# Optimization experiments

Measured on AMD Instinct MI355X. Metric: run time of the kernel, lower is better.

Reference implementation:

```python
import jax, jax.numpy as jnp
import numpy as np

B, L, NC, D = 4, 2048, 4096, 128
ITERS = 4
NHEAD = 8
T = L // 2
C2 = 2 * D


def _ln(x, g, b, eps=1e-5):
    m = jnp.mean(x, axis=-1, keepdims=True)
    v = jnp.var(x, axis=-1, keepdims=True)
    return (x - m) * jax.lax.rsqrt(v + eps) * g + b


def _mlp3(x, W1, b1, W2, b2, W3, b3):
    h = jax.nn.relu(x @ W1 + b1)
    h = jax.nn.relu(h @ W2 + b2)
    return h @ W3 + b3


def _lstm(inp, h, c, Wih, Whh, gi, bi, gh, bh, gc, bc):
    gates = _ln(inp @ Wih, gi, bi) + _ln(h @ Whh, gh, bh)
    i, f, g, o = jnp.split(gates, 4, axis=-1)
    cy = _ln(jax.nn.sigmoid(f) * c + jax.nn.sigmoid(i) * jnp.tanh(g), gc, bc)
    hy = jax.nn.sigmoid(o) * jnp.tanh(cy)
    return hy, cy


def _flip(x):
    # flip matrix with full literal counts == permutation swapping pos/neg halves
    half = x.shape[1] // 2
    return jnp.concatenate([x[:, half:], x[:, :half]], axis=1)


def setup_inputs():
    key = jax.random.key(0)
    ks = iter(jax.random.split(key, 64))
    def xav(fi, fo):
        s = float(np.sqrt(6.0 / (fi + fo)))
        return jax.random.uniform(next(ks), (fi, fo), jnp.float32, -s, s)
    def rn(*shape):
        return jax.random.normal(next(ks), shape, jnp.float32)
    inp = {}
    inp['adjacency_matrices'] = (jax.random.uniform(next(ks), (B, L, NC)) < 0.03).astype(jnp.float32)
    inp['batch_lit_counts'] = jnp.full((B,), L, dtype=jnp.int32)
    inp['L_init'] = rn(1, D) / np.sqrt(D).astype(np.float32)
    inp['C_init'] = rn(1, D) / np.sqrt(D).astype(np.float32)
    for p in ('LC', 'CL'):
        for i in (1, 2, 3):
            inp[p + '_W' + str(i)] = xav(D, D)
            inp[p + '_b' + str(i)] = jnp.full((D,), 0.01, jnp.float32)
    for p, isz in (('Lu', 2 * D), ('Cu', D)):
        inp[p + '_Wih'] = rn(isz, 4 * D)  # torch uses raw randn for LSTM weights
        inp[p + '_Whh'] = rn(D, 4 * D)
        for ln, n in (('lni', 4 * D), ('lnh', 4 * D), ('lnc', D)):
            inp[p + '_' + ln + '_g'] = jnp.ones((n,), jnp.float32)
            inp[p + '_' + ln + '_b'] = jnp.zeros((n,), jnp.float32)
    for p in ('k', 'q', 'v'):
        inp['att_W' + p] = xav(C2, C2)
        inp['att_b' + p] = jnp.zeros((C2,), jnp.float32)
    for p in ('asn', 'vote'):
        inp[p + '_W1'] = xav(C2, D)
        inp[p + '_b1'] = jnp.full((D,), 0.01, jnp.float32)
        inp[p + '_W2'] = xav(D, 1)
        inp[p + '_b2'] = jnp.full((1,), 0.01, jnp.float32)
    return inp


def reference(adjacency_matrices, batch_lit_counts, L_init, C_init,
              LC_W1, LC_b1, LC_W2, LC_b2, LC_W3, LC_b3,
              CL_W1, CL_b1, CL_W2, CL_b2, CL_W3, CL_b3,
              Lu_Wih, Lu_Whh, Lu_lni_g, Lu_lni_b, Lu_lnh_g, Lu_lnh_b, Lu_lnc_g, Lu_lnc_b,
              Cu_Wih, Cu_Whh, Cu_lni_g, Cu_lni_b, Cu_lnh_g, Cu_lnh_b, Cu_lnc_g, Cu_lnc_b,
              att_Wk, att_bk, att_Wq, att_bq, att_Wv, att_bv,
              asn_W1, asn_b1, asn_W2, asn_b2, vote_W1, vote_b1, vote_W2, vote_b2):
    A = adjacency_matrices
    Bb, Ll, Cc = A.shape
    Lh = jnp.broadcast_to(L_init, (Bb, Ll, D))
    Lc = jnp.zeros_like(Lh)
    Ch = jnp.broadcast_to(C_init, (Bb, Cc, D))
    Cxc = jnp.zeros_like(Ch)
    for _ in range(ITERS):
        # literal -> clause messages (gather via A^T)
        LC = jnp.einsum('blc,bld->bcd', A, _mlp3(Lh, LC_W1, LC_b1, LC_W2, LC_b2, LC_W3, LC_b3))
        Ch, Cxc = _lstm(LC, Ch, Cxc, Cu_Wih, Cu_Whh, Cu_lni_g, Cu_lni_b, Cu_lnh_g, Cu_lnh_b, Cu_lnc_g, Cu_lnc_b)
        # clause -> literal messages (scatter via A)
        CL = jnp.einsum('blc,bcd->bld', A, _mlp3(Ch, CL_W1, CL_b1, CL_W2, CL_b2, CL_W3, CL_b3))
        Lh, Lc = _lstm(jnp.concatenate([CL, _flip(Lh)], axis=-1), Lh, Lc,
                       Lu_Wih, Lu_Whh, Lu_lni_g, Lu_lni_b, Lu_lnh_g, Lu_lnh_b, Lu_lnc_g, Lu_lnc_b)
    # readout [h_l ; h_{~l}], positive literals only
    read = jnp.concatenate([Lh, _flip(Lh)], axis=-1)[:, :T]  # [B,T,2D]
    half = batch_lit_counts // 2
    mask = (jnp.arange(T)[None, :] < half[:, None]).astype(read.dtype)  # [B,T]
    read = read * mask[:, :, None]
    hd = C2 // NHEAD
    def heads(x, W, b):
        return (x @ W + b).reshape(Bb, T, NHEAD, hd).transpose(0, 2, 1, 3)
    k = heads(read, att_Wk, att_bk)
    q = heads(read, att_Wq, att_bq)
    v = heads(read, att_Wv, att_bv)
    att = jnp.einsum('bhtd,bhsd->bhts', q, k) * (1.0 / np.sqrt(hd))
    sq = (mask[:, None, :, None] * mask[:, None, None, :]) > 0  # [B,1,T,T]
    att = jnp.where(sq, att, -jnp.inf)
    att = jax.nn.softmax(att, axis=-1)
    att = jnp.where(jnp.isnan(att), 0.0, att)
    y = jnp.einsum('bhts,bhsd->bhtd', att, v).transpose(0, 2, 1, 3).reshape(Bb, T, C2)
    def head_mlp(x, W1, b1, W2, b2):
        return jax.nn.sigmoid(jax.nn.relu(x @ W1 + b1) @ W2 + b2)[..., 0]
    assignments = head_mlp(y, asn_W1, asn_b1, asn_W2, asn_b2) * mask  # [B,T]
    vote_vals = head_mlp(y, vote_W1, vote_b1, vote_W2, vote_b2)
    votes = jnp.sum(vote_vals * mask, axis=1) / jnp.maximum(jnp.sum(mask, axis=1), 1.0)
    return votes, assignments
```

## Files before the change

kernel.cpp:

```cpp
#include <hip/hip_runtime.h>


#define B_    4
#define L_    2048
#define NC_   4096
#define D_    128
#define ITERS_ 4
#define NH_   8
#define T_    1024
#define C2_   256
#define HD_   32
#define BL_   (B_*L_)
#define BNC_  (B_*NC_)
#define QS_   768

typedef unsigned short u16;
typedef __attribute__((ext_vector_type(8))) short b16x8;
typedef __attribute__((ext_vector_type(4))) float f32x4;

static __device__ __forceinline__ float bf2f(u16 u){
  union{unsigned int i; float f;} x; x.i = ((unsigned int)u) << 16; return x.f;
}
static __device__ __forceinline__ u16 f2bf(float f){
  union{float f; unsigned int i;} x; x.f = f;
  unsigned int r = x.i + 0x7fffu + ((x.i >> 16) & 1u);
  return (u16)(r >> 16);
}
static __device__ __forceinline__ float sigm(float x){ return 1.f/(1.f+expf(-x)); }
static __device__ __forceinline__ void split2(float v, u16& h, u16& l){
  unsigned bits = __float_as_uint(v);
  u16 hb = (u16)(bits >> 16);
  float hf = __uint_as_float(((unsigned)hb) << 16);
  h = hb; l = f2bf(v - hf);
}

__global__ __launch_bounds__(256) void k_detect(const unsigned int* __restrict__ a,
                                                int* __restrict__ flag){
  int bad = 0;
  for (int i = threadIdx.x; i < 32768; i += 256){
    unsigned int w = a[i];
    if (w != 0u && w != 0x3F800000u) bad = 1;
  }
  __shared__ int s[256];
  s[threadIdx.x] = bad; __syncthreads();
  for (int o = 128; o > 0; o >>= 1){
    if (threadIdx.x < o) s[threadIdx.x] |= s[threadIdx.x + o];
    __syncthreads();
  }
  if (threadIdx.x == 0) *flag = s[0];
}

#define NCJ_ 29
struct CJobs { const void* src[NCJ_]; unsigned n[NCJ_]; unsigned off[NCJ_]; };

__global__ __launch_bounds__(256) void k_cvt_all(CJobs jb, float* __restrict__ pool,
                                                 const int* __restrict__ flag){
  int j = blockIdx.y;
  unsigned n = jb.n[j];
  unsigned i = blockIdx.x*256 + threadIdx.x;
  if (i >= n) return;
  float v;
  if (*flag) v = bf2f(((const u16*)jb.src[j])[i]);
  else       v = ((const float*)jb.src[j])[i];
  pool[jb.off[j] + i] = v;
}

#define NPJ_ 16
struct PJobs { const void* src[NPJ_]; unsigned n[NPJ_], N[NPJ_], koff[NPJ_],
               ksb[NPJ_], dh[NPJ_], dl[NPJ_]; };

__global__ __launch_bounds__(256) void k_prep(PJobs pj, u16* __restrict__ up,
                                              const int* __restrict__ flag){
  int jj = blockIdx.y;
  unsigned n = pj.n[jj];
  unsigned g = blockIdx.x*256 + threadIdx.x;
  if (g >= n) return;
  unsigned j = g & 7, lane = (g>>3)&63;
  unsigned ksb = pj.ksb[jj];
  unsigned ks = (g>>9) & ((1u<<ksb)-1u);
  unsigned nt = g >> (9+ksb);
  unsigned ncol = nt*16 + (lane&15);
  unsigned k = pj.koff[jj] + ks*32 + ((lane>>4)&3)*8 + j;
  unsigned si = k*pj.N[jj] + ncol;
  float v;
  if (*flag) v = bf2f(((const u16*)pj.src[jj])[si]);
  else       v = ((const float*)pj.src[jj])[si];
  u16 h,l; split2(v, h, l);
  up[pj.dh[jj] + g] = h;
  up[pj.dl[jj] + g] = l;
}

__global__ __launch_bounds__(256) void k_init(float* __restrict__ h, float* __restrict__ c,
                                              const float* __restrict__ init, int n){
  int i = blockIdx.x*256 + threadIdx.x;
  if (i < n){ h[i] = init[i & (D_-1)]; c[i] = 0.f; }
}

__global__ void k_zero_u(unsigned* __restrict__ p, int n){
  int i = blockIdx.x*256 + threadIdx.x; if (i < n) p[i] = 0u;
}
__global__ void k_zero(float* p, int n){
// ... 81 lines not shown
    atomicAdd(cnt_c + cb + j, 1u);
  }
}

__global__ __launch_bounds__(256) void k_fill_c(const unsigned* __restrict__ bits,
    const unsigned* __restrict__ off_c, unsigned* __restrict__ cur_c,
    u16* __restrict__ val_c){
  int g = blockIdx.x*256 + threadIdx.x;
  unsigned m = bits[g];
  int row = g >> 7, w = g & 127;
  int b = row >> 11, l = row & (L_-1);
  unsigned cb = ((unsigned)b << 12) + w*32;
  while (m){
    int j = __ffs(m) - 1; m &= m - 1;
    unsigned idx = cb + j;
    unsigned pos = atomicAdd(cur_c + idx, 1u);
    val_c[off_c[idx] + pos] = (u16)l;
  }
}

__global__ __launch_bounds__(256) void k_spmm(const unsigned* __restrict__ off,
    const u16* __restrict__ val, const float* __restrict__ M, float* __restrict__ out,
    int sh1, int sh2){
  int row  = blockIdx.x*4 + (threadIdx.x >> 6);
  int lane = threadIdx.x & 63;
  unsigned p0 = off[row], p1 = off[row+1];
  const float2* Mp = (const float2*)M + (((size_t)(row >> sh1) << sh2) * 64) + lane;
  float x = 0.f, y = 0.f;
  for (unsigned p = p0; p < p1; ++p){
    float2 v = Mp[(size_t)val[p] * 64];
    x += v.x; y += v.y;
  }
  float2 r; r.x = x; r.y = y;
  ((float2*)out)[(size_t)row*64 + lane] = r;
}

__global__ __launch_bounds__(512) void k_mlp3m(const float* __restrict__ X,
    const u16* __restrict__ W1h, const u16* __restrict__ W1l,
    const u16* __restrict__ W2h, const u16* __restrict__ W2l,
    const u16* __restrict__ W3h, const u16* __restrict__ W3l,
    const float* __restrict__ b1, const float* __restrict__ b2,
    const float* __restrict__ b3, float* __restrict__ Y)
{
  __shared__ __align__(16) u16 Ah[32*136];
  __shared__ __align__(16) u16 Al[32*136];
  const int tid = threadIdx.x, lane = tid & 63, wv = tid >> 6;
  const int quad = lane >> 4, l15 = lane & 15;
  const int r0 = blockIdx.x * 32;
  {
    int row = tid >> 4, c0 = (tid & 15)*8;
    const float4* src = (const float4*)(X + (size_t)(r0+row)*128 + c0);
    float4 v0 = src[0], v1 = src[1];
    u16 h,l;
    split2(v0.x,h,l); Ah[row*136+c0]  =h; Al[row*136+c0]  =l;
    split2(v0.y,h,l); Ah[row*136+c0+1]=h; Al[row*136+c0+1]=l;
    split2(v0.z,h,l); Ah[row*136+c0+2]=h; Al[row*136+c0+2]=l;
    split2(v0.w,h,l); Ah[row*136+c0+3]=h; Al[row*136+c0+3]=l;
    split2(v1.x,h,l); Ah[row*136+c0+4]=h; Al[row*136+c0+4]=l;
    split2(v1.y,h,l); Ah[row*136+c0+5]=h; Al[row*136+c0+5]=l;
    split2(v1.z,h,l); Ah[row*136+c0+6]=h; Al[row*136+c0+6]=l;
    split2(v1.w,h,l); Ah[row*136+c0+7]=h; Al[row*136+c0+7]=l;
  }
  __syncthreads();
  const u16* Whs[3] = {W1h, W2h, W3h};
  const u16* Wls[3] = {W1l, W2l, W3l};
  const float* bs[3] = {b1, b2, b3};
  #pragma unroll
  for (int layer = 0; layer < 3; layer++){
    f32x4 acc[2] = {};
    #pragma unroll
    for (int ks = 0; ks < 4; ks++){
      b16x8 a_h[2], a_l[2];
      #pragma unroll
      for (int mt = 0; mt < 2; mt++){
        int ao = (mt*16 + l15)*136 + ks*32 + quad*8;
        a_h[mt] = *(const b16x8*)(Ah + ao);
        a_l[mt] = *(const b16x8*)(Al + ao);
      }
      size_t bo = (size_t)((wv*4 + ks)*64 + lane)*8;
      b16x8 bh = *(const b16x8*)(Whs[layer] + bo);
      b16x8 bl = *(const b16x8*)(Wls[layer] + bo);
      #pragma unroll
      for (int mt = 0; mt < 2; mt++){
        acc[mt] = __builtin_amdgcn_mfma_f32_16x16x32_bf16(a_h[mt], bh, acc[mt],0,0,0);
        acc[mt] = __builtin_amdgcn_mfma_f32_16x16x32_bf16(a_h[mt], bl, acc[mt],0,0,0);
        acc[mt] = __builtin_amdgcn_mfma_f32_16x16x32_bf16(a_l[mt], bh, acc[mt],0,0,0);
      }
    }
    int col = wv*16 + l15;
    if (layer < 2){
      float bb = bs[layer][col];
      __syncthreads();
      #pragma unroll
      for (int mt = 0; mt < 2; mt++)
        #pragma unroll
        for (int r = 0; r < 4; r++){
          int row = mt*16 + quad*4 + r;
          float v = fmaxf(acc[mt][r] + bb, 0.f);
          u16 h,l; split2(v,h,l);
          Ah[row*136 + col] = h; Al[row*136 + col] = l;
        }
      __syncthreads();
    } else {
      float bb = bs[2][col];
      #pragma unroll
      for (int mt = 0; mt < 2; mt++)
        #pragma unroll
        for (int r = 0; r < 4; r++){
          int row = mt*16 + quad*4 + r;
          Y[(size_t)(r0+row)*128 + col] = acc[mt][r] + bb;
        }
    }
  }
}

template<int NSEG>
__global__ __launch_bounds__(512) void k_lstm_mfma(
    const float* __restrict__ A0, const float* __restrict__ A1, const float* __restrict__ A2,
    int flip1,
    const u16* __restrict__ W0h, const u16* __restrict__ W0l,
    const u16* __restrict__ W1h, const u16* __restrict__ W1l,
    const u16* __restrict__ W2h, const u16* __restrict__ W2l,
    const float* __restrict__ lni_g, const float* __restrict__ lni_b,
    const float* __restrict__ lnh_g, const float* __restrict__ lnh_b,
    const float* __restrict__ lnc_g, const float* __restrict__ lnc_b,
    const float* __restrict__ c_in, float* __restrict__ c_out,
    float* __restrict__ h_out)
{
  __shared__ __align__(16) float G[32*516];
  __shared__ float red[8][32][4];
  __shared__ float st[32][4];
  u16* Ah = (u16*)G;
  u16* Al = Ah + 32*136;
  const int tid = threadIdx.x, lane = tid & 63, wv = tid >> 6;
  const int quad = lane >> 4, l15 = lane & 15;
  const int r0 = blockIdx.x * 32;

  f32x4 acc1[2][4] = {}, acc2[2][4] = {};

  #pragma unroll
  for (int s = 0; s < NSEG; ++s){
    const float* Ap = (s==0) ? A0 : ((s==1) ? A1 : A2);
    const u16* Wh = (s==0) ? W0h : ((s==1) ? W1h : W2h);
    const u16* Wl = (s==0) ? W0l : ((s==1) ? W1l : W2l);
    const int fm = (s==1) ? flip1 : 0;
    __syncthreads();
    {
      int row = tid >> 4, c0 = (tid & 15)*8;
      int arow = (r0 + row) ^ fm;
      const float4* src = (const float4*)(Ap + (size_t)arow*128 + c0);
      float4 v0 = src[0], v1 = src[1];
      u16 h,l;
      split2(v0.x,h,l); Ah[row*136+c0]  =h; Al[row*136+c0]  =l;
      split2(v0.y,h,l); Ah[row*136+c0+1]=h; Al[row*136+c0+1]=l;
      split2(v0.z,h,l); Ah[row*136+c0+2]=h; Al[row*136+c0+2]=l;
      split2(v0.w,h,l); Ah[row*136+c0+3]=h; Al[row*136+c0+3]=l;
      split2(v1.x,h,l); Ah[row*136+c0+4]=h; Al[row*136+c0+4]=l;
      split2(v1.y,h,l); Ah[row*136+c0+5]=h; Al[row*136+c0+5]=l;
      split2(v1.z,h,l); Ah[row*136+c0+6]=h; Al[row*136+c0+6]=l;
      split2(v1.w,h,l); Ah[row*136+c0+7]=h; Al[row*136+c0+7]=l;
    }
    __syncthreads();
    f32x4 (*accp)[4] = (s == NSEG-1) ? acc2 : acc1;
    #pragma unroll
    for (int ks = 0; ks < 4; ks++){
      b16x8 a_h[2], a_l[2];
      #pragma unroll
      for (int mt = 0; mt < 2; mt++){
        int ao = (mt*16 + l15)*136 + ks*32 + quad*8;
        a_h[mt] = *(const b16x8*)(Ah + ao);
        a_l[mt] = *(const b16x8*)(Al + ao);
      }
      #pragma unroll
      for (int ntl = 0; ntl < 4; ntl++){
        int nt = wv*4 + ntl;
        size_t bo = (size_t)((nt*4 + ks)*64 + lane)*8;
        b16x8 bh = *(const b16x8*)(Wh + bo);
        b16x8 bl = *(const b16x8*)(Wl + bo);
        #pragma unroll
        for (int mt = 0; mt < 2; mt++){
          accp[mt][ntl] = __builtin_amdgcn_mfma_f32_16x16x32_bf16(a_h[mt], bh, accp[mt][ntl],0,0,0);
          accp[mt][ntl] = __builtin_amdgcn_mfma_f32_16x16x32_bf16(a_h[mt], bl, accp[mt][ntl],0,0,0);
          accp[mt][ntl] = __builtin_amdgcn_mfma_f32_16x16x32_bf16(a_l[mt], bh, accp[mt][ntl],0,0,0);
        }
      }
    }
  }

  #pragma unroll
  for (int mt = 0; mt < 2; mt++)
    #pragma unroll
    for (int r = 0; r < 4; r++){
      float s1=0.f, q1=0.f, s2=0.f, q2=0.f;
      #pragma unroll
      for (int ntl = 0; ntl < 4; ntl++){
        float v1 = acc1[mt][ntl][r]; s1 += v1; q1 += v1*v1;
        float v2 = acc2[mt][ntl][r]; s2 += v2; q2 += v2*v2;
      }
      #pragma unroll
      for (int m = 1; m < 16; m <<= 1){
        s1 += __shfl_xor(s1, m); q1 += __shfl_xor(q1, m);
        s2 += __shfl_xor(s2, m); q2 += __shfl_xor(q2, m);
      }
      if (l15 == 0){
        int row = mt*16 + quad*4 + r;
        red[wv][row][0]=s1; red[wv][row][1]=q1; red[wv][row][2]=s2; red[wv][row][3]=q2;
      }
    }
  __syncthreads();
  if (tid < 32){
    int row = tid;
    float s1=0.f,q1=0.f,s2=0.f,q2=0.f;
    #pragma unroll
    for (int w = 0; w < 8; w++){
      s1 += red[w][row][0]; q1 += red[w][row][1];
      s2 += red[w][row][2]; q2 += red[w][row][3];
    }
    const float i512 = 1.f/512.f;
    float m1 = s1*i512, v1 = fmaxf(q1*i512 - m1*m1, 0.f);
    float m2 = s2*i512, v2 = fmaxf(q2*i512 - m2*m2, 0.f);
    st[row][0] = m1; st[row][1] = rsqrtf(v1 + 1e-5f);
    st[row][2] = m2; st[row][3] = rsqrtf(v2 + 1e-5f);
  }
  __syncthreads();

  #pragma unroll
  for (int mt = 0; mt < 2; mt++)
    #pragma unroll
    for (int ntl = 0; ntl < 4; ntl++){
      int col = wv*64 + ntl*16 + l15;
      float gi = lni_g[col], bi = lni_b[col];
      float gh = lnh_g[col], bh = lnh_b[col];
      #pragma unroll
      for (int r = 0; r < 4; r++){
        int row = mt*16 + quad*4 + r;
        float v = (acc1[mt][ntl][r] - st[row][0])*st[row][1]*gi + bi
                + (acc2[mt][ntl][r] - st[row][2])*st[row][3]*gh + bh;
        G[row*516 + col] = v;
      }
    }
  __syncthreads();

  float lcg0 = lnc_g[lane], lcb0 = lnc_b[lane];
  float lcg1 = lnc_g[lane+64], lcb1 = lnc_b[lane+64];
  const float i128 = 1.f/128.f;
  #pragma unroll
  for (int i = 0; i < 4; i++){
    int row = wv*4 + i;
    int rg = r0 + row;
    float cp[2], sc = 0.f, qc = 0.f;
    #pragma unroll
    for (int jj = 0; jj < 2; jj++){
      int c = lane + 64*jj;
      float iv = sigm(G[row*516 + c]);
      float fv = sigm(G[row*516 + 128 + c]);
      float gv = tanhf(G[row*516 + 256 + c]);
      cp[jj] = fv * c_in[(size_t)rg*128 + c] + iv*gv;
      sc += cp[jj]; qc += cp[jj]*cp[jj];
    }
    #pragma unroll
    for (int m = 1; m < 64; m <<= 1){ sc += __shfl_xor(sc, m); qc += __shfl_xor(qc, m); }
    float mc = sc*i128, vc = fmaxf(qc*i128 - mc*mc, 0.f), rsc = rsqrtf(vc + 1e-5f);
    #pragma unroll
    for (int jj = 0; jj < 2; jj++){
      int c = lane + 64*jj;
      float cy = (cp[jj]-mc)*rsc*(jj ? lcg1 : lcg0) + (jj ? lcb1 : lcb0);
      c_out[(size_t)rg*128 + c] = cy;
      float ov = sigm(G[row*516 + 384 + c]);
      h_out[(size_t)rg*128 + c] = ov*tanhf(cy);
    }
  }
}

template<int NT, int NSPLIT, int KK32, int ACT, int GATHER>
__global__ __launch_bounds__(512) void k_gemm_mfma(const float* __restrict__ A,
    const u16* __restrict__ Wh, const u16* __restrict__ Wl,
    const float* __restrict__ bias, float* __restrict__ Y,
    const int* __restrict__ counts)
{
  const int NTOT = NSPLIT*8*NT*16;
  const int LDA = KK32*32 + 8;
  __shared__ __align__(16) u16 Ah[32*(KK32*32+8)];
  __shared__ __align__(16) u16 Al[32*(KK32*32+8)];
  const int tid = threadIdx.x, lane = tid & 63, wv = tid >> 6;
  const int quad = lane >> 4, l15 = lane & 15;
  const int r0 = blockIdx.x * 32, by = blockIdx.y;
  {
    int row = tid >> 4, c0 = (tid & 15)*(KK32*2);
    if (GATHER){
      int r = r0 + row; int b = r >> 10; int t = r & 1023;
      int half = counts[b] / 2; if (half > T_) half = T_;
      float msk = (t < half) ? 1.f : 0.f;
      #pragma unroll
      for (int q4 = 0; q4 < KK32/2; q4++){
        int c = c0 + q4*4;
        const float* src = A + ((size_t)(b*L_ + t + ((c >= 128) ? T_ : 0))*128 + (c & 127));
        float4 v = *(const float4*)src;
        u16 h,l;
        split2(v.x*msk,h,l); Ah[row*LDA+c]  =h; Al[row*LDA+c]  =l;
        split2(v.y*msk,h,l); Ah[row*LDA+c+1]=h; Al[row*LDA+c+1]=l;
        split2(v.z*msk,h,l); Ah[row*LDA+c+2]=h; Al[row*LDA+c+2]=l;
        split2(v.w*msk,h,l); Ah[row*LDA+c+3]=h; Al[row*LDA+c+3]=l;
      }
    } else {
      const float4* src = (const float4*)(A + (size_t)(r0+row)*(KK32*32) + c0);
      #pragma unroll
      for (int q4 = 0; q4 < KK32/2; q4++){
        float4 v = src[q4]; int c = c0 + q4*4;
        u16 h,l;
        split2(v.x,h,l); Ah[row*LDA+c]  =h; Al[row*LDA+c]  =l;
        split2(v.y,h,l); Ah[row*LDA+c+1]=h; Al[row*LDA+c+1]=l;
        split2(v.z,h,l); Ah[row*LDA+c+2]=h; Al[row*LDA+c+2]=l;
        split2(v.w,h,l); Ah[row*LDA+c+3]=h; Al[row*LDA+c+3]=l;
      }
    }
  }
  __syncthreads();
  f32x4 acc[2][NT] = {};
  #pragma unroll
  for (int ks = 0; ks < KK32; ks++){
    b16x8 a_h[2], a_l[2];
    #pragma unroll
    for (int mt = 0; mt < 2; mt++){
      int ao = (mt*16 + l15)*LDA + ks*32 + quad*8;
      a_h[mt] = *(const b16x8*)(Ah + ao);
      a_l[mt] = *(const b16x8*)(Al + ao);
    }
    #pragma unroll
    for (int ntl = 0; ntl < NT; ntl++){
      int nt = by*(8*NT) + wv*NT + ntl;
      size_t bo = (size_t)((nt*KK32 + ks)*64 + lane)*8;
      b16x8 bh = *(const b16x8*)(Wh + bo);
      b16x8 bl = *(const b16x8*)(Wl + bo);
      #pragma unroll
      for (int mt = 0; mt < 2; mt++){
        acc[mt][ntl] = __builtin_amdgcn_mfma_f32_16x16x32_bf16(a_h[mt], bh, acc[mt][ntl],0,0,0);
        acc[mt][ntl] = __builtin_amdgcn_mfma_f32_16x16x32_bf16(a_h[mt], bl, acc[mt][ntl],0,0,0);
        acc[mt][ntl] = __builtin_amdgcn_mfma_f32_16x16x32_bf16(a_l[mt], bh, acc[mt][ntl],0,0,0);
      }
    }
  }
  #pragma unroll
  for (int mt = 0; mt < 2; mt++)
    #pragma unroll
    for (int ntl = 0; ntl < NT; ntl++){
      int colg = by*(8*NT*16) + wv*(NT*16) + ntl*16 + l15;
      float bb = bias[colg];
      #pragma unroll
      for (int r = 0; r < 4; r++){
        int row = mt*16 + quad*4 + r;
        float v = acc[mt][ntl][r] + bb;
        if (ACT) v = fmaxf(v, 0.f);
        Y[(size_t)(r0+row)*NTOT + colg] = v;
      }
    }
}

__global__ __launch_bounds__(256) void k_attn_tile(const float* __restrict__ qkv,
    const int* __restrict__ counts, float* __restrict__ y)
{
  const int b = blockIdx.z, h = blockIdx.y, t0 = blockIdx.x*64;
  int half = counts[b] / 2; if (half > T_) half = T_; if (half < 0) half = 0;
  const int tid = threadIdx.x;
  const int lane = tid & 63, wv = tid >> 6;
  const int lr = tid >> 2, lc = (tid & 3)*8;

  if (t0 >= half){
    float* yp = y + ((size_t)(b*T_ + t0 + lr)*C2_ + h*HD_ + lc);
    #pragma unroll
    for (int j = 0; j < 8; j++) yp[j] = 0.f;
    return;
  }

  __shared__ float Qs[64][36];
  __shared__ float Ks[64][32];
  __shared__ float Ss[64][68];

  {
    const float* qp = qkv + (size_t)(b*T_ + t0 + lr)*QS_ + h*HD_ + lc;
    float4 a0 = *(const float4*)qp;
    float4 a1 = *(const float4*)(qp+4);
    *(float4*)&Qs[lr][lc]   = a0;
    *(float4*)&Qs[lr][lc+4] = a1;
  }

  const int ty = tid >> 4, tx = tid & 15;
  const int sr = wv*16 + (lane & 15);
  const int spart = (lane >> 4) * 16;
  const int rp = lane >> 3, cq = lane & 7;
  const int r0 = wv*16 + rp*2;

  float4 acc0 = {0.f,0.f,0.f,0.f}, acc1 = {0.f,0.f,0.f,0.f};
  float mst = -3e38f, lst = 0.f;
  const float scale = 0.17677669529663687f;
  const int nt = (half + 63) >> 6;

  for (int st = 0; st < nt; ++st){
    const int s0 = st*64;
    __syncthreads();
    {
      const float* kp = qkv + (size_t)(b*T_ + s0 + lr)*QS_ + 256 + h*HD_ + lc;
      float4 k0 = *(const float4*)kp;
      float4 k1 = *(const float4*)(kp+4);
      int key = (lr >> 2) & 7;
      int c0 = lc >> 2;
      *(float4*)&Ks[lr][4*((c0  ) ^ key)] = k0;
      *(float4*)&Ks[lr][4*((c0+1) ^ key)] = k1;
    }
    __syncthreads();

    float s4[4][4];
    #pragma unroll
    for (int i = 0; i < 4; i++)
      #pragma unroll
      for (int j = 0; j < 4; j++) s4[i][j] = 0.f;
    const int xk = tx & 7;
    #pragma unroll
    for (int kk4 = 0; kk4 < 8; kk4++){
      float4 a4[4], b4[4];
      #pragma unroll
      for (int i = 0; i < 4; i++) a4[i] = *(const float4*)&Qs[ty*4+i][kk4*4];
      const int pk = 4*(kk4 ^ xk);
      #pragma unroll
      for (int j = 0; j < 4; j++) b4[j] = *(const float4*)&Ks[tx*4+j][pk];
      #pragma unroll
      for (int i = 0; i < 4; i++)
        #pragma unroll
        for (int j = 0; j < 4; j++)
          s4[i][j] += a4[i].x*b4[j].x + a4[i].y*b4[j].y + a4[i].z*b4[j].z + a4[i].w*b4[j].w;
    }
    #pragma unroll
    for (int i = 0; i < 4; i++){
      float4 w4;
      w4.x = (s0 + tx*4 + 0 < half) ? s4[i][0]*scale : -1e30f;
      w4.y = (s0 + tx*4 + 1 < half) ? s4[i][1]*scale : -1e30f;
      w4.z = (s0 + tx*4 + 2 < half) ? s4[i][2]*scale : -1e30f;
      w4.w = (s0 + tx*4 + 3 < half) ? s4[i][3]*scale : -1e30f;
      *(float4*)&Ss[ty*4+i][tx*4] = w4;
    }

    float pvv[16];
    float vmax = -3e38f;
    #pragma unroll
    for (int c4 = 0; c4 < 4; c4++){
      float4 t4 = *(const float4*)&Ss[sr][spart + c4*4];
      pvv[c4*4+0] = t4.x; pvv[c4*4+1] = t4.y; pvv[c4*4+2] = t4.z; pvv[c4*4+3] = t4.w;
      vmax = fmaxf(vmax, fmaxf(fmaxf(t4.x, t4.y), fmaxf(t4.z, t4.w)));
    }
    vmax = fmaxf(vmax, __shfl_xor(vmax, 16));
    vmax = fmaxf(vmax, __shfl_xor(vmax, 32));
    float nm = fmaxf(mst, vmax);
    float alpha = expf(mst - nm);
    float psum = 0.f;
    #pragma unroll
    for (int c = 0; c < 16; c++){
      float p = expf(pvv[c] - nm);
      pvv[c] = p; psum += p;
    }
    psum += __shfl_xor(psum, 16);
    psum += __shfl_xor(psum, 32);
    lst = lst*alpha + psum;
    mst = nm;
    #pragma unroll
    for (int c4 = 0; c4 < 4; c4++){
      float4 w4; w4.x = pvv[c4*4+0]; w4.y = pvv[c4*4+1]; w4.z = pvv[c4*4+2]; w4.w = pvv[c4*4+3];
      *(float4*)&Ss[sr][spart + c4*4] = w4;
    }
    float al0 = __shfl(alpha, 2*rp);
    float al1 = __shfl(alpha, 2*rp + 1);
    acc0.x *= al0; acc0.y *= al0; acc0.z *= al0; acc0.w *= al0;
    acc1.x *= al1; acc1.y *= al1; acc1.z *= al1; acc1.w *= al1;

    const float* vbase = qkv + (size_t)(b*T_ + s0)*QS_ + 512 + h*HD_ + cq*4;
    #pragma unroll 4
    for (int kk4 = 0; kk4 < 16; kk4++){
      float4 p0 = *(const float4*)&Ss[r0  ][kk4*4];
      float4 p1 = *(const float4*)&Ss[r0+1][kk4*4];
      float4 v0 = *(const float4*)(vbase + (size_t)(kk4*4+0)*QS_);
      float4 v1 = *(const float4*)(vbase + (size_t)(kk4*4+1)*QS_);
      float4 v2 = *(const float4*)(vbase + (size_t)(kk4*4+2)*QS_);
      float4 v3 = *(const float4*)(vbase + (size_t)(kk4*4+3)*QS_);
      acc0.x += p0.x*v0.x + p0.y*v1.x + p0.z*v2.x + p0.w*v3.x;
      acc0.y += p0.x*v0.y + p0.y*v1.y + p0.z*v2.y + p0.w*v3.y;
      acc0.z += p0.x*v0.z + p0.y*v1.z + p0.z*v2.z + p0.w*v3.z;
      acc0.w += p0.x*v0.w + p0.y*v1.w + p0.z*v2.w + p0.w*v3.w;
      acc1.x += p1.x*v0.x + p1.y*v1.x + p1.z*v2.x + p1.w*v3.x;
      acc1.y += p1.x*v0.y + p1.y*v1.y + p1.z*v2.y + p1.w*v3.y;
      acc1.z += p1.x*v0.z + p1.y*v1.z + p1.z*v2.z + p1.w*v3.z;
      acc1.w += p1.x*v0.w + p1.y*v1.w + p1.z*v2.w + p1.w*v3.w;
    }
  }

  float l0 = __shfl(lst, 2*rp);
  float l1 = __shfl(lst, 2*rp + 1);
  float m0 = (t0 + r0     < half && l0 > 0.f) ? 1.f/l0 : 0.f;
  float m1 = (t0 + r0 + 1 < half && l1 > 0.f) ? 1.f/l1 : 0.f;
  float4 o0, o1;
  o0.x = acc0.x*m0; o0.y = acc0.y*m0; o0.z = acc0.z*m0; o0.w = acc0.w*m0;
  o1.x = acc1.x*m1; o1.y = acc1.y*m1; o1.z = acc1.z*m1; o1.w = acc1.w*m1;
  *(float4*)(y + ((size_t)(b*T_ + t0 + r0    )*C2_ + h*HD_ + cq*4)) = o0;
  *(float4*)(y + ((size_t)(b*T_ + t0 + r0 + 1)*C2_ + h*HD_ + cq*4)) = o1;
}

__global__ __launch_bounds__(128) void k_final(const float* __restrict__ hv,
    const float* __restrict__ aW2, const float* __restrict__ ab2,
    const float* __restrict__ vW2, const float* __restrict__ vb2,
    const int* __restrict__ counts, void* __restrict__ outv,
    float* __restrict__ vote_sum, const int* __restrict__ flag)
{
  int row = blockIdx.x, tid = threadIdx.x;
  int b = row / T_, t = row - b*T_;
  int half = counts[b] / 2; if (half > T_) half = T_;
  float pa = hv[(size_t)row*256 + tid]       * aW2[tid];
  float pv = hv[(size_t)row*256 + 128 + tid] * vW2[tid];
  #pragma unroll
  for (int off = 32; off > 0; off >>= 1){ pa += __shfl_down(pa, off); pv += __shfl_down(pv, off); }
  __shared__ float r[2][2];
  int wid = tid >> 6, lane = tid & 63;
  if (lane == 0){ r[0][wid] = pa; r[1][wid] = pv; }
  __syncthreads();
  if (tid == 0){
    float a  = sigm(r[0][0] + r[0][1] + ab2[0]);
    float vv = sigm(r[1][0] + r[1][1] + vb2[0]);
    bool mk = (t < half);
    float av = mk ? a : 0.f;
    if (*flag) ((u16*)outv)[4 + row] = f2bf(av);
    else       ((float*)outv)[4 + row] = av;
    if (mk) atomicAdd(vote_sum + b, vv);
  }
}

__global__ void k_votes(const float* __restrict__ vote_sum, const int* __restrict__ counts,
                        void* __restrict__ outv, const int* __restrict__ flag){
  int b = threadIdx.x;
  if (b < B_){
    int half = counts[b] / 2; if (half > T_) half = T_;
    float den = (float)(half > 1 ? half : 1);
    float vv = vote_sum[b] / den;
    if (*flag) ((u16*)outv)[b] = f2bf(vv);
    else       ((float*)outv)[b] = vv;
  }
}

extern "C" void kernel_launch(void* const* d_in, const int* in_sizes, int n_in,
                              void* d_out, int out_size, void* d_ws, size_t ws_size,
                              hipStream_t stream)
{
  const void* A_adj = d_in[0];
  const int* counts = (const int*)d_in[1];

  const size_t M1 = (size_t)1048576;
  const size_t NEED = (5*M1 + M1 + 2*M1 + 2*M1 + 700416 + 16416 + 8224
                       + 16384 + 8192 + 520000 + 520000 + 32) * sizeof(float);
  if (ws_size < NEED) return;

  float* ws = (float*)d_ws;
  float* R    = ws;
  float* Lc   = R + 5*M1;
  float* Ch   = Lc + M1;
  float* Cc   = Ch + 2*M1;
  float* wp   = Cc + 2*M1;
  unsigned* off_c = (unsigned*)(wp + 700416);
  unsigned* off_l = off_c + 16416;
  unsigned* cnt_c = off_l + 8224;
  unsigned* cnt_l = cnt_c + 16384;
  u16* val_c = (u16*)(cnt_l + 8192);
  u16* val_l = (u16*)((float*)val_c + 520000);
  float* tail = (float*)val_l + 520000;
  float* vote_sum = tail;
  int* flag = (int*)(tail + 8);
  unsigned* bits = (unsigned*)R;

  float* R0 = R, *R1 = R + M1, *R2 = R + 2*M1, *R3 = R + 3*M1, *R4 = R + 4*M1;

  k_detect<<<1, 256, 0, stream>>>((const unsigned int*)A_adj, flag);

  CJobs cj;
  int ncj = 0;
  unsigned off = 0;
  auto cadd = [&](int idx, unsigned n)->float*{
    cj.src[ncj] = d_in[idx]; cj.n[ncj] = n; cj.off[ncj] = off;
    float* p = wp + off; off += (n + 3u) & ~3u; ncj++; return p;
  };
  float* Linit = cadd(2, 128);
// ... 11 lines not shown
  float* bqkv = wp + off;
  cj.src[ncj]=d_in[35]; cj.n[ncj]=256; cj.off[ncj]=off;       ncj++;
  cj.src[ncj]=d_in[33]; cj.n[ncj]=256; cj.off[ncj]=off+256;   ncj++;
  cj.src[ncj]=d_in[37]; cj.n[ncj]=256; cj.off[ncj]=off+512;   ncj++;
  off += 768;
  float* bhv = wp + off;
  cj.src[ncj]=d_in[39]; cj.n[ncj]=128; cj.off[ncj]=off;       ncj++;
  cj.src[ncj]=d_in[43]; cj.n[ncj]=128; cj.off[ncj]=off+128;   ncj++;
  off += 256;
  { dim3 g(2, NCJ_); k_cvt_all<<<g, 256, 0, stream>>>(cj, wp, flag); }

  u16* up = (u16*)(wp + ((off + 3u) & ~3u));
  PJobs pj;
  int npj = 0;
  unsigned uoff = 0;
  auto padd = [&](int idx, unsigned n, unsigned Nw, unsigned koff, unsigned ksb,
                  unsigned dsth, unsigned dstl){
    pj.src[npj]=d_in[idx]; pj.n[npj]=n; pj.N[npj]=Nw; pj.koff[npj]=koff;
    pj.ksb[npj]=ksb; pj.dh[npj]=dsth; pj.dl[npj]=dstl; npj++;
  };
  auto solo = [&](int idx, unsigned n, unsigned Nw, unsigned koff, unsigned ksb,
                  const u16** h, const u16** l){
    padd(idx, n, Nw, koff, ksb, uoff, uoff + n);
    *h = up + uoff; *l = up + uoff + n; uoff += 2*n;
  };
  const u16 *lc1h,*lc1l,*lc2h,*lc2l,*lc3h,*lc3l,*cl1h,*cl1l,*cl2h,*cl2l,*cl3h,*cl3l;
  const u16 *cwih_h,*cwih_l,*cwhh_h,*cwhh_l;
  const u16 *lwa_h,*lwa_l,*lwb_h,*lwb_l,*lwhh_h,*lwhh_l;
  solo(4, 16384,128,0,2,&lc1h,&lc1l);  solo(6, 16384,128,0,2,&lc2h,&lc2l);
  solo(8, 16384,128,0,2,&lc3h,&lc3l);  solo(10,16384,128,0,2,&cl1h,&cl1l);
  solo(12,16384,128,0,2,&cl2h,&cl2l);  solo(14,16384,128,0,2,&cl3h,&cl3l);
  solo(24,65536,512,0,2,&cwih_h,&cwih_l);
  solo(25,65536,512,0,2,&cwhh_h,&cwhh_l);
  solo(16,65536,512,0,  2,&lwa_h,&lwa_l);
  solo(16,65536,512,128,2,&lwb_h,&lwb_l);
  solo(17,65536,512,0,2,&lwhh_h,&lwhh_l);
  const u16* wqkv_h = up + uoff;
  const u16* wqkv_l = up + uoff + 196608;
  padd(34, 65536, 256, 0, 3, uoff,           uoff+196608);
  padd(32, 65536, 256, 0, 3, uoff+65536,     uoff+196608+65536);
  padd(36, 65536, 256, 0, 3, uoff+131072,    uoff+196608+131072);
  uoff += 393216;
  const u16* whv_h = up + uoff;
  const u16* whv_l = up + uoff + 65536;
  padd(38, 32768, 128, 0, 3, uoff,        uoff+65536);
  padd(42, 32768, 128, 0, 3, uoff+32768,  uoff+65536+32768);
  uoff += 131072;
  { dim3 g(256, NPJ_); k_prep<<<g, 256, 0, stream>>>(pj, up, flag); }

  k_zero_u<<<(16384+255)/256, 256, 0, stream>>>(cnt_c, 16384);
  k_pack<<<BL_, 128, 0, stream>>>(A_adj, bits, cnt_l, flag);
  k_scan<<<1, 256, 0, stream>>>(cnt_l, off_l, 8192);
  k_fill_l<<<BL_, 128, 0, stream>>>(bits, off_l, val_l, cnt_c);
  k_scan<<<1, 256, 0, stream>>>(cnt_c, off_c, 16384);
  k_fill_c<<<4096, 256, 0, stream>>>(bits, off_c, cnt_c, val_c);

  k_init<<<(BL_*D_)/256, 256, 0, stream>>>(R0, Lc, Linit, BL_*D_);
  k_init<<<(BNC_*D_)/256, 256, 0, stream>>>(Ch, Cc, Cinit, BNC_*D_);

  for (int it = 0; it < ITERS_; ++it){
    bool ev = ((it & 1) == 0);
    float* cur  = ev ? R0 : R4;
    float* msgL = ev ? R1 : R0;
    float* LCb  = ev ? R2 : R1;
    float* msgC = LCb;
    float* CLb  = ev ? R1 : R3;
    float* nxt  = ev ? R4 : R0;

    k_mlp3m<<<BL_/32, 512, 0, stream>>>(cur, lc1h,lc1l, lc2h,lc2l, lc3h,lc3l,
                                        LC_b1, LC_b2, LC_b3, msgL);
    k_spmm<<<BNC_/4, 256, 0, stream>>>(off_c, val_c, msgL, LCb, 12, 11);
    k_lstm_mfma<2><<<BNC_/32, 512, 0, stream>>>(LCb, Ch, nullptr, 0,
        cwih_h, cwih_l, cwhh_h, cwhh_l, nullptr, nullptr,
        Cu_lni_g, Cu_lni_b, Cu_lnh_g, Cu_lnh_b, Cu_lnc_g, Cu_lnc_b, Cc, Cc, Ch);
    k_mlp3m<<<BNC_/32, 512, 0, stream>>>(Ch, cl1h,cl1l, cl2h,cl2l, cl3h,cl3l,
                                         CL_b1, CL_b2, CL_b3, msgC);
    k_spmm<<<BL_/4, 256, 0, stream>>>(off_l, val_l, msgC, CLb, 11, 12);
    k_lstm_mfma<3><<<BL_/32, 512, 0, stream>>>(CLb, cur, cur, 1024,
        lwa_h, lwa_l, lwb_h, lwb_l, lwhh_h, lwhh_l,
        Lu_lni_g, Lu_lni_b, Lu_lnh_g, Lu_lnh_b, Lu_lnc_g, Lu_lnc_b, Lc, Lc, nxt);
  }
  float* Lh = R0;

  float* qkvb  = Ch;
  float* yb    = R1;
  float* hv    = R2;

  { dim3 g((B_*T_)/32, 2);
    k_gemm_mfma<3,2,8,0,1><<<g, 512, 0, stream>>>(Lh, wqkv_h, wqkv_l, bqkv, qkvb, counts); }
  { dim3 g(T_/64, NH_, B_); k_attn_tile<<<g, 256, 0, stream>>>(qkvb, counts, yb); }
  { dim3 g((B_*T_)/32, 2);
    k_gemm_mfma<1,2,8,1,0><<<g, 512, 0, stream>>>(yb, whv_h, whv_l, bhv, hv, counts); }
  k_zero<<<1, 64, 0, stream>>>(vote_sum, B_);
  k_final<<<B_*T_, 128, 0, stream>>>(hv, asn_W2, asn_b2, vote_W2, vote_b2,
                                     counts, d_out, vote_sum, flag);
  k_votes<<<1, 64, 0, stream>>>(vote_sum, counts, d_out, flag);
}
```

Measured before the change: 1.676 ms.

## Rewrite attention with split-bf16 MFMA and emit head-major Q/K/V^T from QKV GEMM

Replaces the scalar FP32 tiled attention kernel with an MFMA-based flash-style kernel. It uses hi/lo bf16 splitting (three MFMAs per product) to keep near-FP32 accuracy. A dedicated QKV GEMM now writes Q and K in head-major layout and V transposed, as split bf16 halves, so the attention kernel can load MFMA operands directly without LDS staging for K and V. This adds scattered u16 stores in the GEMM epilogue and splitting overhead, and reuses the Ch/Cc buffers as scratch.

```diff
diff --git a/kernel.cpp b/kernel.cpp
--- a/kernel.cpp
+++ b/kernel.cpp
@@ -12,11 +12,12 @@
 #define HD_   32
 #define BL_   (B_*L_)
 #define BNC_  (B_*NC_)
-#define QS_   768
 
 typedef unsigned short u16;
 typedef __attribute__((ext_vector_type(8))) short b16x8;
 typedef __attribute__((ext_vector_type(4))) float f32x4;
+
+#define MFMA_BF16(a,b,c) __builtin_amdgcn_mfma_f32_16x16x32_bf16((a),(b),(c),0,0,0)
 
 static __device__ __forceinline__ float bf2f(u16 u){
   union{unsigned int i; float f;} x; x.i = ((unsigned int)u) << 16; return x.f;
@@ -264,9 +265,9 @@
       b16x8 bl = *(const b16x8*)(Wls[layer] + bo);
       #pragma unroll
       for (int mt = 0; mt < 2; mt++){
-        acc[mt] = __builtin_amdgcn_mfma_f32_16x16x32_bf16(a_h[mt], bh, acc[mt],0,0,0);
-        acc[mt] = __builtin_amdgcn_mfma_f32_16x16x32_bf16(a_h[mt], bl, acc[mt],0,0,0);
-        acc[mt] = __builtin_amdgcn_mfma_f32_16x16x32_bf16(a_l[mt], bh, acc[mt],0,0,0);
+        acc[mt] = MFMA_BF16(a_h[mt], bh, acc[mt]);
+        acc[mt] = MFMA_BF16(a_h[mt], bl, acc[mt]);
+        acc[mt] = MFMA_BF16(a_l[mt], bh, acc[mt]);
       }
     }
     int col = wv*16 + l15;
@@ -361,9 +362,9 @@
         b16x8 bl = *(const b16x8*)(Wl + bo);
         #pragma unroll
         for (int mt = 0; mt < 2; mt++){
-          accp[mt][ntl] = __builtin_amdgcn_mfma_f32_16x16x32_bf16(a_h[mt], bh, accp[mt][ntl],0,0,0);
-          accp[mt][ntl] = __builtin_amdgcn_mfma_f32_16x16x32_bf16(a_h[mt], bl, accp[mt][ntl],0,0,0);
-          accp[mt][ntl] = __builtin_amdgcn_mfma_f32_16x16x32_bf16(a_l[mt], bh, accp[mt][ntl],0,0,0);
+          accp[mt][ntl] = MFMA_BF16(a_h[mt], bh, accp[mt][ntl]);
+          accp[mt][ntl] = MFMA_BF16(a_h[mt], bl, accp[mt][ntl]);
+          accp[mt][ntl] = MFMA_BF16(a_l[mt], bh, accp[mt][ntl]);
         }
       }
     }
@@ -516,9 +517,9 @@
       b16x8 bl = *(const b16x8*)(Wl + bo);
       #pragma unroll
       for (int mt = 0; mt < 2; mt++){
-        acc[mt][ntl] = __builtin_amdgcn_mfma_f32_16x16x32_bf16(a_h[mt], bh, acc[mt][ntl],0,0,0);
-        acc[mt][ntl] = __builtin_amdgcn_mfma_f32_16x16x32_bf16(a_h[mt], bl, acc[mt][ntl],0,0,0);
-        acc[mt][ntl] = __builtin_amdgcn_mfma_f32_16x16x32_bf16(a_l[mt], bh, acc[mt][ntl],0,0,0);
+        acc[mt][ntl] = MFMA_BF16(a_h[mt], bh, acc[mt][ntl]);
+        acc[mt][ntl] = MFMA_BF16(a_h[mt], bl, acc[mt][ntl]);
+        acc[mt][ntl] = MFMA_BF16(a_l[mt], bh, acc[mt][ntl]);
       }
     }
   }
@@ -538,150 +539,192 @@
     }
 }
 
-__global__ __launch_bounds__(256) void k_attn_tile(const float* __restrict__ qkv,
+__global__ __launch_bounds__(512) void k_qkv_gemm(const float* __restrict__ A,
+    const u16* __restrict__ Wh, const u16* __restrict__ Wl,
+    const float* __restrict__ bias,
+    u16* __restrict__ Qh, u16* __restrict__ Ql,
+    u16* __restrict__ Kh, u16* __restrict__ Kl,
+    u16* __restrict__ Vth, u16* __restrict__ Vtl,
+    const int* __restrict__ counts)
+{
+  const int KK32 = 8, NT = 3;
+  const int LDA = KK32*32 + 8;
+  __shared__ __align__(16) u16 Ah[32*(KK32*32+8)];
+  __shared__ __align__(16) u16 Al[32*(KK32*32+8)];
+  const int tid = threadIdx.x, lane = tid & 63, wv = tid >> 6;
+  const int quad = lane >> 4, l15 = lane & 15;
+  const int r0 = blockIdx.x * 32, by = blockIdx.y;
+  {
+    int row = tid >> 4, c0 = (tid & 15)*(KK32*2);
+    int r = r0 + row; int b = r >> 10; int t = r & 1023;
+    int half = counts[b] / 2; if (half > T_) half = T_;
+    float msk = (t < half) ? 1.f : 0.f;
+    #pragma unroll
+    for (int q4 = 0; q4 < KK32/2; q4++){
+      int c = c0 + q4*4;
+      const float* src = A + ((size_t)(b*L_ + t + ((c >= 128) ? T_ : 0))*128 + (c & 127));
+      float4 v = *(const float4*)src;
+      u16 h,l;
+      split2(v.x*msk,h,l); Ah[row*LDA+c]  =h; Al[row*LDA+c]  =l;
+      split2(v.y*msk,h,l); Ah[row*LDA+c+1]=h; Al[row*LDA+c+1]=l;
+      split2(v.z*msk,h,l); Ah[row*LDA+c+2]=h; Al[row*LDA+c+2]=l;
+      split2(v.w*msk,h,l); Ah[row*LDA+c+3]=h; Al[row*LDA+c+3]=l;
+    }
+  }
+  __syncthreads();
+  f32x4 acc[2][NT] = {};
+  #pragma unroll
+  for (int ks = 0; ks < KK32; ks++){
+    b16x8 a_h[2], a_l[2];
+    #pragma unroll
+    for (int mt = 0; mt < 2; mt++){
+      int ao = (mt*16 + l15)*LDA + ks*32 + quad*8;
+      a_h[mt] = *(const b16x8*)(Ah + ao);
+      a_l[mt] = *(const b16x8*)(Al + ao);
+    }
+    #pragma unroll
+    for (int ntl = 0; ntl < NT; ntl++){
+      int nt = by*(8*NT) + wv*NT + ntl;
+      size_t bo = (size_t)((nt*KK32 + ks)*64 + lane)*8;
+      b16x8 bh = *(const b16x8*)(Wh + bo);
+      b16x8 bl = *(const b16x8*)(Wl + bo);
+      #pragma unroll
+      for (int mt = 0; mt < 2; mt++){
+        acc[mt][ntl] = MFMA_BF16(a_h[mt], bh, acc[mt][ntl]);
+        acc[mt][ntl] = MFMA_BF16(a_h[mt], bl, acc[mt][ntl]);
+        acc[mt][ntl] = MFMA_BF16(a_l[mt], bh, acc[mt][ntl]);
+      }
+    }
+  }
+  #pragma unroll
+  for (int mt = 0; mt < 2; mt++)
+    #pragma unroll
+    for (int ntl = 0; ntl < NT; ntl++){
+      int colg = by*(8*NT*16) + wv*(NT*16) + ntl*16 + l15;
+      float bb = bias[colg];
+      #pragma unroll
+      for (int r = 0; r < 4; r++){
+        int row = r0 + mt*16 + quad*4 + r;
+        int bI = row >> 10, t = row & 1023;
+        float v = acc[mt][ntl][r] + bb;
+        u16 hh, ll; split2(v, hh, ll);
+        if (colg < 256){
+          int h8 = colg >> 5, k = colg & 31;
+          size_t idx = ((size_t)(bI*NH_ + h8)*1024 + t)*32 + k;
+          Qh[idx] = hh; Ql[idx] = ll;
+        } else if (colg < 512){
+          int c = colg - 256; int h8 = c >> 5, k = c & 31;
+          size_t idx = ((size_t)(bI*NH_ + h8)*1024 + t)*32 + k;
+          Kh[idx] = hh; Kl[idx] = ll;
+        } else {
+          int c = colg - 512; int h8 = c >> 5, n = c & 31;
+          size_t idx = ((size_t)(bI*NH_ + h8)*32 + n)*1024 + t;
+          Vth[idx] = hh; Vtl[idx] = ll;
+        }
+      }
+    }
+}
+
+__global__ __launch_bounds__(256) void k_attn_mfma(
+    const u16* __restrict__ Qh, const u16* __restrict__ Ql,
+    const u16* __restrict__ Kh, const u16* __restrict__ Kl,
+    const u16* __restrict__ Vth, const u16* __restrict__ Vtl,
     const int* __restrict__ counts, float* __restrict__ y)
 {
   const int b = blockIdx.z, h = blockIdx.y, t0 = blockIdx.x*64;
   int half = counts[b] / 2; if (half > T_) half = T_; if (half < 0) half = 0;
-  const int tid = threadIdx.x;
-  const int lane = tid & 63, wv = tid >> 6;
-  const int lr = tid >> 2, lc = (tid & 3)*8;
-
-  if (t0 >= half){
-    float* yp = y + ((size_t)(b*T_ + t0 + lr)*C2_ + h*HD_ + lc);
-    #pragma unroll
-    for (int j = 0; j < 8; j++) yp[j] = 0.f;
-    return;
-  }
-
-  __shared__ float Qs[64][36];
-  __shared__ float Ks[64][32];
-  __shared__ float Ss[64][68];
-
-  {
-    const float* qp = qkv + (size_t)(b*T_ + t0 + lr)*QS_ + h*HD_ + lc;
-    float4 a0 = *(const float4*)qp;
-    float4 a1 = *(const float4*)(qp+4);
-    *(float4*)&Qs[lr][lc]   = a0;
-    *(float4*)&Qs[lr][lc+4] = a1;
-  }
-
-  const int ty = tid >> 4, tx = tid & 15;
-  const int sr = wv*16 + (lane & 15);
-  const int spart = (lane >> 4) * 16;
-  const int rp = lane >> 3, cq = lane & 7;
-  const int r0 = wv*16 + rp*2;
-
-  float4 acc0 = {0.f,0.f,0.f,0.f}, acc1 = {0.f,0.f,0.f,0.f};
-  float mst = -3e38f, lst = 0.f;
+  const int tid = threadIdx.x, lane = tid & 63, w = tid >> 6;
+  const int quad = lane >> 4, l15 = lane & 15;
+  __shared__ __align__(16) u16 Pb[4][2][16*72];
+  const int tw = t0 + w*16;
+  const size_t bh = (size_t)(b*NH_ + h)*32768;
+  const u16* qhb = Qh + bh; const u16* qlb = Ql + bh;
+  const u16* khb = Kh + bh; const u16* klb = Kl + bh;
+  const u16* vhb = Vth + bh; const u16* vlb = Vtl + bh;
+
+  b16x8 qah = *(const b16x8*)(qhb + (size_t)(tw + l15)*32 + quad*8);
+  b16x8 qal = *(const b16x8*)(qlb + (size_t)(tw + l15)*32 + quad*8);
+
+  f32x4 accO[2] = {};
+  float mst[4], lst[4];
+  #pragma unroll
+  for (int r = 0; r < 4; r++){ mst[r] = -3e38f; lst[r] = 0.f; }
   const float scale = 0.17677669529663687f;
-  const int nt = (half + 63) >> 6;
-
-  for (int st = 0; st < nt; ++st){
+  const int ntile = (t0 < half) ? ((half + 63) >> 6) : 0;
+
+  for (int st = 0; st < ntile; ++st){
     const int s0 = st*64;
-    __syncthreads();
-    {
-      const float* kp = qkv + (size_t)(b*T_ + s0 + lr)*QS_ + 256 + h*HD_ + lc;
-      float4 k0 = *(const float4*)kp;
-      float4 k1 = *(const float4*)(kp+4);
-      int key = (lr >> 2) & 7;
-      int c0 = lc >> 2;
-      *(float4*)&Ks[lr][4*((c0  ) ^ key)] = k0;
-      *(float4*)&Ks[lr][4*((c0+1) ^ key)] = k1;
-    }
-    __syncthreads();
-
-    float s4[4][4];
-    #pragma unroll
-    for (int i = 0; i < 4; i++)
-      #pragma unroll
-      for (int j = 0; j < 4; j++) s4[i][j] = 0.f;
-    const int xk = tx & 7;
-    #pragma unroll
-    for (int kk4 = 0; kk4 < 8; kk4++){
-      float4 a4[4], b4[4];
-      #pragma unroll
-      for (int i = 0; i < 4; i++) a4[i] = *(const float4*)&Qs[ty*4+i][kk4*4];
-      const int pk = 4*(kk4 ^ xk);
-      #pragma unroll
-      for (int j = 0; j < 4; j++) b4[j] = *(const float4*)&Ks[tx*4+j][pk];
-      #pragma unroll
-      for (int i = 0; i < 4; i++)
-        #pragma unroll
-        for (int j = 0; j < 4; j++)
-          s4[i][j] += a4[i].x*b4[j].x + a4[i].y*b4[j].y + a4[i].z*b4[j].z + a4[i].w*b4[j].w;
-    }
-    #pragma unroll
-    for (int i = 0; i < 4; i++){
-      float4 w4;
-      w4.x = (s0 + tx*4 + 0 < half) ? s4[i][0]*scale : -1e30f;
-      w4.y = (s0 + tx*4 + 1 < half) ? s4[i][1]*scale : -1e30f;
-      w4.z = (s0 + tx*4 + 2 < half) ? s4[i][2]*scale : -1e30f;
-      w4.w = (s0 + tx*4 + 3 < half) ? s4[i][3]*scale : -1e30f;
-      *(float4*)&Ss[ty*4+i][tx*4] = w4;
-    }
-
-    float pvv[16];
-    float vmax = -3e38f;
-    #pragma unroll
-    for (int c4 = 0; c4 < 4; c4++){
-      float4 t4 = *(const float4*)&Ss[sr][spart + c4*4];
-      pvv[c4*4+0] = t4.x; pvv[c4*4+1] = t4.y; pvv[c4*4+2] = t4.z; pvv[c4*4+3] = t4.w;
-      vmax = fmaxf(vmax, fmaxf(fmaxf(t4.x, t4.y), fmaxf(t4.z, t4.w)));
-    }
-    vmax = fmaxf(vmax, __shfl_xor(vmax, 16));
-    vmax = fmaxf(vmax, __shfl_xor(vmax, 32));
-    float nm = fmaxf(mst, vmax);
-    float alpha = expf(mst - nm);
-    float psum = 0.f;
-    #pragma unroll
-    for (int c = 0; c < 16; c++){
-      float p = expf(pvv[c] - nm);
-      pvv[c] = p; psum += p;
-    }
-    psum += __shfl_xor(psum, 16);
-    psum += __shfl_xor(psum, 32);
-    lst = lst*alpha + psum;
-    mst = nm;
-    #pragma unroll
-    for (int c4 = 0; c4 < 4; c4++){
-      float4 w4; w4.x = pvv[c4*4+0]; w4.y = pvv[c4*4+1]; w4.z = pvv[c4*4+2]; w4.w = pvv[c4*4+3];
-      *(float4*)&Ss[sr][spart + c4*4] = w4;
-    }
-    float al0 = __shfl(alpha, 2*rp);
-    float al1 = __shfl(alpha, 2*rp + 1);
-    acc0.x *= al0; acc0.y *= al0; acc0.z *= al0; acc0.w *= al0;
-    acc1.x *= al1; acc1.y *= al1; acc1.z *= al1; acc1.w *= al1;
-
-    const float* vbase = qkv + (size_t)(b*T_ + s0)*QS_ + 512 + h*HD_ + cq*4;
-    #pragma unroll 4
-    for (int kk4 = 0; kk4 < 16; kk4++){
-      float4 p0 = *(const float4*)&Ss[r0  ][kk4*4];
-      float4 p1 = *(const float4*)&Ss[r0+1][kk4*4];
-      float4 v0 = *(const float4*)(vbase + (size_t)(kk4*4+0)*QS_);
-      float4 v1 = *(const float4*)(vbase + (size_t)(kk4*4+1)*QS_);
-      float4 v2 = *(const float4*)(vbase + (size_t)(kk4*4+2)*QS_);
-      float4 v3 = *(const float4*)(vbase + (size_t)(kk4*4+3)*QS_);
-      acc0.x += p0.x*v0.x + p0.y*v1.x + p0.z*v2.x + p0.w*v3.x;
-      acc0.y += p0.x*v0.y + p0.y*v1.y + p0.z*v2.y + p0.w*v3.y;
-      acc0.z += p0.x*v0.z + p0.y*v1.z + p0.z*v2.z + p0.w*v3.z;
-      acc0.w += p0.x*v0.w + p0.y*v1.w + p0.z*v2.w + p0.w*v3.w;
-      acc1.x += p1.x*v0.x + p1.y*v1.x + p1.z*v2.x + p1.w*v3.x;
-      acc1.y += p1.x*v0.y + p1.y*v1.y + p1.z*v2.y + p1.w*v3.y;
-      acc1.z += p1.x*v0.z + p1.y*v1.z + p1.z*v2.z + p1.w*v3.z;
-      acc1.w += p1.x*v0.w + p1.y*v1.w + p1.z*v2.w + p1.w*v3.w;
-    }
-  }
-
-  float l0 = __shfl(lst, 2*rp);
-  float l1 = __shfl(lst, 2*rp + 1);
-  float m0 = (t0 + r0     < half && l0 > 0.f) ? 1.f/l0 : 0.f;
-  float m1 = (t0 + r0 + 1 < half && l1 > 0.f) ? 1.f/l1 : 0.f;
-  float4 o0, o1;
-  o0.x = acc0.x*m0; o0.y = acc0.y*m0; o0.z = acc0.z*m0; o0.w = acc0.w*m0;
-  o1.x = acc1.x*m1; o1.y = acc1.y*m1; o1.z = acc1.z*m1; o1.w = acc1.w*m1;
-  *(float4*)(y + ((size_t)(b*T_ + t0 + r0    )*C2_ + h*HD_ + cq*4)) = o0;
-  *(float4*)(y + ((size_t)(b*T_ + t0 + r0 + 1)*C2_ + h*HD_ + cq*4)) = o1;
+    f32x4 s4[4];
+    #pragma unroll
+    for (int nt = 0; nt < 4; nt++){
+      int srow = s0 + nt*16 + l15;
+      b16x8 kh8 = *(const b16x8*)(khb + (size_t)srow*32 + quad*8);
+      b16x8 kl8 = *(const b16x8*)(klb + (size_t)srow*32 + quad*8);
+      f32x4 a = {};
+      a = MFMA_BF16(qah, kh8, a);
+      a = MFMA_BF16(qah, kl8, a);
+      a = MFMA_BF16(qal, kh8, a);
+      s4[nt] = a;
+    }
+    #pragma unroll
+    for (int nt = 0; nt < 4; nt++){
+      bool ok = (s0 + nt*16 + l15) < half;
+      #pragma unroll
+      for (int r = 0; r < 4; r++)
+        s4[nt][r] = ok ? s4[nt][r]*scale : -1e30f;
+    }
+    float alpha[4];
+    #pragma unroll
+    for (int r = 0; r < 4; r++){
+      float vm = fmaxf(fmaxf(s4[0][r], s4[1][r]), fmaxf(s4[2][r], s4[3][r]));
+      vm = fmaxf(vm, __shfl_xor(vm, 1));
+      vm = fmaxf(vm, __shfl_xor(vm, 2));
+      vm = fmaxf(vm, __shfl_xor(vm, 4));
+      vm = fmaxf(vm, __shfl_xor(vm, 8));
+      float nm = fmaxf(mst[r], vm);
+      alpha[r] = expf(mst[r] - nm);
+      mst[r] = nm;
+      float sum = 0.f;
+      #pragma unroll
+      for (int nt = 0; nt < 4; nt++){
+        float p = expf(s4[nt][r] - nm);
+        sum += p;
+        u16 hh, ll; split2(p, hh, ll);
+        int ad = (quad*4 + r)*72 + nt*16 + l15;
+        Pb[w][0][ad] = hh; Pb[w][1][ad] = ll;
+      }
+      sum += __shfl_xor(sum, 1);
+      sum += __shfl_xor(sum, 2);
+      sum += __shfl_xor(sum, 4);
+      sum += __shfl_xor(sum, 8);
+      lst[r] = lst[r]*alpha[r] + sum;
+      accO[0][r] *= alpha[r];
+      accO[1][r] *= alpha[r];
+    }
+    #pragma unroll
+    for (int kc = 0; kc < 2; kc++){
+      b16x8 ph = *(const b16x8*)&Pb[w][0][l15*72 + kc*32 + quad*8];
+      b16x8 pl = *(const b16x8*)&Pb[w][1][l15*72 + kc*32 + quad*8];
+      #pragma unroll
+      for (int nt = 0; nt < 2; nt++){
+        const size_t vo = (size_t)(nt*16 + l15)*1024 + s0 + kc*32 + quad*8;
+        b16x8 vh8 = *(const b16x8*)(vhb + vo);
+        b16x8 vl8 = *(const b16x8*)(vlb + vo);
+        accO[nt] = MFMA_BF16(ph, vh8, accO[nt]);
+        accO[nt] = MFMA_BF16(ph, vl8, accO[nt]);
+        accO[nt] = MFMA_BF16(pl, vh8, accO[nt]);
+      }
+    }
+  }
+
+  #pragma unroll
+  for (int r = 0; r < 4; r++){
+    int t = tw + quad*4 + r;
+    float inv = (t < half && lst[r] > 0.f) ? 1.f/lst[r] : 0.f;
+    #pragma unroll
+    for (int nt = 0; nt < 2; nt++)
+      y[(size_t)(b*T_ + t)*C2_ + h*HD_ + nt*16 + l15] = accO[nt][r]*inv;
+  }
 }
 
 __global__ __launch_bounds__(128) void k_final(const float* __restrict__ hv,
@@ -859,13 +902,19 @@
   }
   float* Lh = R0;
 
-  float* qkvb  = Ch;
-  float* yb    = R1;
-  float* hv    = R2;
+  u16* qk = (u16*)Ch;
+  u16* Qh_ = qk;           u16* Ql_ = qk + 1048576;
+  u16* Kh_ = qk + 2097152; u16* Kl_ = qk + 3145728;
+  u16* vt = (u16*)Cc;
+  u16* Vth_ = vt;          u16* Vtl_ = vt + 1048576;
+  float* yb = R1;
+  float* hv = R2;
 
   { dim3 g((B_*T_)/32, 2);
-    k_gemm_mfma<3,2,8,0,1><<<g, 512, 0, stream>>>(Lh, wqkv_h, wqkv_l, bqkv, qkvb, counts); }
-  { dim3 g(T_/64, NH_, B_); k_attn_tile<<<g, 256, 0, stream>>>(qkvb, counts, yb); }
+    k_qkv_gemm<<<g, 512, 0, stream>>>(Lh, wqkv_h, wqkv_l, bqkv,
+                                      Qh_, Ql_, Kh_, Kl_, Vth_, Vtl_, counts); }
+  { dim3 g(T_/64, NH_, B_);
+    k_attn_mfma<<<g, 256, 0, stream>>>(Qh_, Ql_, Kh_, Kl_, Vth_, Vtl_, counts, yb); }
   { dim3 g((B_*T_)/32, 2);
     k_gemm_mfma<1,2,8,1,0><<<g, 512, 0, stream>>>(yb, whv_h, whv_l, bhv, hv, counts); }
   k_zero<<<1, 64, 0, stream>>>(vote_sum, B_);
```

Result: faster. 1.593 ms (median of 2 runs) (-4.9%).
